# Kernel optimization log

Measured on AMD Instinct MI355X. Metric: run time of the kernel, lower is better.

## Reference

```python
import jax, jax.numpy as jnp
import numpy as np

N, E, B = 10000, 25000, 128
NF, EF, D = 32, 8, 64
STEPS = 3   # message passing steps
S2S = 3     # set2set processing steps
EPS = 1e-5

def setup_inputs() -> dict:
    key = jax.random.key(0)
    ks = jax.random.split(key, 32)
    g = lambda i, shape, scale=0.05: (jax.random.normal(ks[i], shape, dtype=jnp.float32) * scale)
    inp = {
        'x': jax.random.normal(ks[0], (N, NF), dtype=jnp.float32),
        'edge_index': jax.random.randint(ks[1], (2, E), 0, N, dtype=jnp.int32),
        'edge_attr': jax.random.normal(ks[2], (E, EF), dtype=jnp.float32),
        'batch': jnp.sort(jax.random.randint(ks[3], (N,), 0, B, dtype=jnp.int32)),
        # dense0
        'W0': g(4, (NF, D)), 'b0': jnp.zeros((D,), jnp.float32),
        # edge MLP: EF -> 2D -> D*D
        'We1': g(5, (EF, 2 * D)), 'be1': jnp.zeros((2 * D,), jnp.float32),
        'We2': g(6, (2 * D, D * D)), 'be2': jnp.zeros((D * D,), jnp.float32),
        # NNConv root weight + bias
        'root': g(7, (D, D)), 'conv_b': jnp.zeros((D,), jnp.float32),
        # GRU (input D, hidden D); gate order r, z, n (torch layout)
        'Wi': g(8, (D, 3 * D)), 'bi': jnp.zeros((3 * D,), jnp.float32),
        'Wh': g(9, (D, 3 * D)), 'bh': jnp.zeros((3 * D,), jnp.float32),
        # Set2Set LSTM (input 2D, hidden D); gate order i, f, g, o
        'Wli': g(10, (2 * D, 4 * D)), 'bli': jnp.zeros((4 * D,), jnp.float32),
        'Wlh': g(11, (D, 4 * D)), 'blh': jnp.zeros((4 * D,), jnp.float32),
        'Wr1': g(12, (2 * D, D)), 'br1': jnp.zeros((D,), jnp.float32),
        'gamma': jnp.ones((D,), jnp.float32), 'beta': jnp.zeros((D,), jnp.float32),
        'Wr2': g(13, (D, 1)), 'br2': jnp.zeros((1,), jnp.float32),
    }
    return inp

def _forward(x, edge_index, edge_attr, batch, W0, b0, We1, be1, We2, be2,
             root, conv_b, Wi, bi, Wh, bh, Wli, bli, Wlh, blh,
             Wr1, br1, gamma, beta, Wr2, br2):
    src, dst = edge_index[0], edge_index[1]
    out = jax.nn.relu(x @ W0 + b0)            # [N, D]
    h = out                                    # GRU hidden (seq_len=1)
    # edge-conditioned weights depend only on edge_attr -> compute once
    ew = (jax.nn.relu(edge_attr @ We1 + be1) @ We2 + be2).reshape(E, D, D)
    deg = jnp.maximum(jax.ops.segment_sum(jnp.ones((E,), x.dtype), dst, num_segments=N), 1.0)
    for _ in range(STEPS):
        msg = jnp.einsum('ed,edf->ef', out[src], ew)               # [E, D]
        agg = jax.ops.segment_sum(msg, dst, num_segments=N) / deg[:, None]
        m = jax.nn.relu(agg + out @ root + conv_b)                  # NNConv + relu
        # GRU cell
        gi = m @ Wi + bi
        gh = h @ Wh + bh
        ir, iz, ig = jnp.split(gi, 3, axis=-1)
        hr, hz, hg = jnp.split(gh, 3, axis=-1)
        r = jax.nn.sigmoid(ir + hr)
        z = jax.nn.sigmoid(iz + hz)
        n = jnp.tanh(ig + r * hg)
        h = (1.0 - z) * n + z * h
        out = h
    # Set2Set readout
    q_star = jnp.zeros((B, 2 * D), x.dtype)
    hl = jnp.zeros((B, D), x.dtype)
    cl = jnp.zeros((B, D), x.dtype)
    for _ in range(S2S):
        gates = q_star @ Wli + bli + hl @ Wlh + blh
        ig_, fg_, gg_, og_ = jnp.split(gates, 4, axis=-1)
        cl = jax.nn.sigmoid(fg_) * cl + jax.nn.sigmoid(ig_) * jnp.tanh(gg_)
        hl = jax.nn.sigmoid(og_) * jnp.tanh(cl)
        q = hl                                                      # [B, D]
        e = jnp.sum(out * q[batch], axis=-1)                        # [N]
        emax = jax.ops.segment_max(e, batch, num_segments=B)
        a = jnp.exp(e - emax[batch])
        a = a / jnp.maximum(jax.ops.segment_sum(a, batch, num_segments=B), 1e-12)[batch]
        r_read = jax.ops.segment_sum(a[:, None] * out, batch, num_segments=B)  # [B, D]
        q_star = jnp.concatenate([q, r_read], axis=-1)
    y = q_star @ Wr1 + br1
    mu = jnp.mean(y, axis=0)
    var = jnp.mean((y - mu) ** 2, axis=0)
    y = (y - mu) * jax.lax.rsqrt(var + EPS) * gamma + beta
    y = jax.nn.relu(y)
    y = y @ Wr2 + br2
    return y.reshape(-1)                                            # [B]

def reference(x, edge_index, edge_attr, batch, W0, b0, We1, be1, We2, be2,
              root, conv_b, Wi, bi, Wh, bh, Wli, bli, Wlh, blh,
              Wr1, br1, gamma, beta, Wr2, br2):
    return _forward(x, edge_index, edge_attr, batch, W0, b0, We1, be1, We2, be2,
                    root, conv_b, Wi, bi, Wh, bh, Wli, bli, Wlh, blh,
                    Wr1, br1, gamma, beta, Wr2, br2)
```

## Files before the change

### kernel.cpp

```cpp
#include <hip/hip_runtime.h>
#include <hip/hip_bf16.h>

constexpr int kN = 10000;
constexpr int kE = 25000;
constexpr int kB = 128;
constexpr int kNF = 32;
constexpr int kEF = 8;
constexpr int kD = 64;
constexpr int kGrp = 392;
constexpr int kEPad = kGrp * 64;
constexpr int kNCap = 320;

typedef __attribute__((ext_vector_type(8))) short short8;
typedef __attribute__((ext_vector_type(4))) float floatx4;
typedef __attribute__((ext_vector_type(16))) float floatx16;
typedef _Float16 half8 __attribute__((ext_vector_type(8)));

union HU { uint4 u; half8 h; short8 s; };

__device__ __forceinline__ unsigned short f2h(float f) {
  union { _Float16 h; unsigned short u; } cv;
  cv.h = (_Float16)f;
  return cv.u;
}
__device__ __forceinline__ unsigned pkrtz(float lo, float hi) {
  unsigned r;
  asm("v_cvt_pkrtz_f16_f32 %0, %1, %2" : "=v"(r) : "v"(lo), "v"(hi));
  return r;
}
__device__ __forceinline__ float sigmf(float x) { return 1.f / (1.f + __expf(-x)); }
__device__ __forceinline__ float tanh_(float x) { return 1.f - 2.f / (__expf(2.f * x) + 1.f); }

constexpr int kBlkDense = 2500;
constexpr int kBlkHid   = 12544;
constexpr int kBlkPrep  = 258;
constexpr int kBlkDeg   = 98;
constexpr int kB0H = kBlkDense;
constexpr int kB0P = kB0H + kBlkHid;
constexpr int kB0G = kB0P + kBlkPrep;
constexpr int kB0B = kB0G + kBlkDeg;
constexpr int kBlkSetup = kB0B + 1;

__global__ __launch_bounds__(256) void k_setup(
    const float* __restrict__ x, const float* __restrict__ W0, const float* __restrict__ b0,
    const float* __restrict__ ea, const float* __restrict__ We1, const float* __restrict__ be1,
    const float* __restrict__ We2, const float* __restrict__ be2,
    const int* __restrict__ ei, const int* __restrict__ batch,
    float* __restrict__ outn, unsigned short* __restrict__ hid7,
    unsigned short* __restrict__ Bc2, float* __restrict__ deg, int* __restrict__ start) {
  const int blk = blockIdx.x, t = threadIdx.x;
  if (blk < kB0H) {
    int gid = blk * 256 + t;
    int n = gid >> 6, f = gid & 63;
    float acc = b0[f];
    const float* xr = x + n * kNF;
#pragma unroll
    for (int j = 0; j < kNF; ++j) acc += xr[j] * W0[j * kD + f];
    outn[gid] = fmaxf(acc, 0.f);
  } else if (blk < kB0P) {
    int gid = (blk - kB0H) * 256 + t;
    int e_loc = gid & 63, h = (gid >> 6) & 127, grp = gid >> 13;
    int e = grp * 64 + e_loc;
    float r = 0.f;
    if (e < kE) {
      float acc = be1[h];
      const float* er = ea + e * kEF;
#pragma unroll
      for (int j = 0; j < kEF; ++j) acc += er[j] * We1[j * 128 + h];
      r = fmaxf(acc, 0.f);
    }
    hid7[gid] = f2h(r);
  } else if (blk < kB0G) {
    int lg = (blk - kB0P) * 256 + t;
    int lane = lg & 63, slot = lg >> 6;
    int fcol, dbase;
    const float* srcmat;
    if (slot < 1024) {
      int nf_ = slot & 1, hdb = slot >> 1;
      int db = hdb & 3, h = hdb >> 2;
      fcol = nf_ * 32 + (lane & 31);
      dbase = db * 16 + (lane >> 5) * 8;
      srcmat = We2 + (size_t)h * 4096;
    } else {
      int s = slot - 1024;
      int db = s >> 1, nf_ = s & 1;
      fcol = nf_ * 32 + (lane & 31);
      dbase = db * 16 + (lane >> 5) * 8;
      srcmat = be2;
    }
    unsigned short v[8];
#pragma unroll
    for (int j = 0; j < 8; ++j) v[j] = f2h(srcmat[(size_t)(dbase + j) * 64 + fcol]);
    *(short8*)(Bc2 + (size_t)slot * 512 + lane * 8) = *(short8*)v;
  } else if (blk < kB0B) {
    int e = (blk - kB0G) * 256 + t;
    if (e < kE) atomicAdd(&deg[ei[kE + e]], 1.f);
  } else {
    if (t > kB) return;
    int lo = 0, hi = kN;
    while (lo < hi) { int mid = (lo + hi) >> 1; if (batch[mid] < t) lo = mid + 1; else hi = mid; }
    start[t] = lo;
  }
}

__global__ __launch_bounds__(256) void k_csr(const float* __restrict__ deg,
                                             int* __restrict__ ptr) {
  __shared__ int ps[256];
  int t = threadIdx.x;
  int base = t * 40;
  int s = 0;
#pragma unroll 8
  for (int j = 0; j < 40; ++j) {
    int n = base + j;
    if (n < kN) s += (int)deg[n];
  }
  ps[t] = s;
  __syncthreads();
  for (int off = 1; off < 256; off <<= 1) {
    int v = (t >= off) ? ps[t - off] : 0;
    __syncthreads();
    ps[t] += v;
    __syncthreads();
  }
  int run = ps[t] - s;
  for (int j = 0; j < 40; ++j) {
    int n = base + j;
    if (n < kN) { ptr[n] = run; run += (int)deg[n]; }
  }
  if (t == 255) ptr[kN] = ps[255];
}

__global__ __launch_bounds__(256) void k_scatter(const int* __restrict__ ei,
    const int* __restrict__ ptr, int* __restrict__ cnt, int* __restrict__ perm) {
  int e = blockIdx.x * 256 + threadIdx.x;
  if (e < kE) {
    int d = ei[kE + e];
    int pos = atomicAdd(&cnt[d], 1);
    perm[e] = ptr[d] + pos;
  }
}

__global__ __launch_bounds__(256) void k_msgA(const int* __restrict__ ei,
    const float* __restrict__ outn, const unsigned short* __restrict__ hid7,
    const unsigned short* __restrict__ Bc2, const int* __restrict__ perm,
    float* __restrict__ msg0, float* __restrict__ msg1) {
  __shared__ __align__(16) unsigned short hidS[64 * 64];
  __shared__ __align__(16) float res[4][32 * 64];
  const int t = threadIdx.x, lane = t & 63, wave = t >> 6;
  const int er = lane & 31, hi5 = lane >> 5;
  const int grp = blockIdx.x, by = blockIdx.y, e0 = grp * 64;
  float* __restrict__ msgP = by ? msg1 : msg0;
  {
    const char* hsrc = (const char*)(hid7 + (size_t)grp * 8192 + by * 4096);
#pragma unroll
    for (int i = 0; i < 2; ++i) {
      int off = (wave * 2 + i) * 1024 + lane * 16;
      __builtin_amdgcn_global_load_lds(
          (const __attribute__((address_space(1))) void*)(hsrc + off),
          (__attribute__((address_space(3))) void*)((char*)hidS + off), 16, 0, 0);
    }
  }
  const int hg0 = by * 64 + wave * 16;
  const unsigned short* bp = Bc2 + (size_t)(hg0 * 8) * 512 + lane * 8;
  short8 bvr[8];
#pragma unroll
  for (int j = 0; j < 8; ++j) bvr[j] = *(const short8*)(bp + (size_t)j * 512);
  HU o8[2][4];
#pragma unroll
  for (int mf = 0; mf < 2; ++mf) {
    int e = e0 + mf * 32 + er;
    int s = (e < kE) ? ei[e] : 0;
    const float* base = outn + (size_t)s * 64 + hi5 * 8;
#pragma unroll
    for (int db = 0; db < 4; ++db) {
      floatx4 q0 = *(const floatx4*)(base + db * 16);
      floatx4 q1 = *(const floatx4*)(base + db * 16 + 4);
      o8[mf][db].u = (uint4){pkrtz(q0.x, q0.y), pkrtz(q0.z, q0.w),
                             pkrtz(q1.x, q1.y), pkrtz(q1.z, q1.w)};
    }
  }
  __syncthreads();

  floatx16 acc[2][2];
#pragma unroll
  for (int mf = 0; mf < 2; ++mf)
#pragma unroll
    for (int nf = 0; nf < 2; ++nf)
#pragma unroll
      for (int i = 0; i < 16; ++i) acc[mf][nf][i] = 0.f;

  const int hl0 = wave * 16;
#pragma unroll 2
  for (int hh = 0; hh < 16; ++hh) {
    int hl = hl0 + hh;
    unsigned p0 = (unsigned)hidS[hl * 64 + er] * 0x10001u;
    unsigned p1 = (unsigned)hidS[hl * 64 + 32 + er] * 0x10001u;
    HU hv0, hv1;
    hv0.u = (uint4){p0, p0, p0, p0};
    hv1.u = (uint4){p1, p1, p1, p1};
    const unsigned short* bpn = bp + (size_t)((hh + 1) * 8) * 512;
#pragma unroll
    for (int db = 0; db < 4; ++db) {
      HU bv0, bv1;
      bv0.s = bvr[db * 2]; bv1.s = bvr[db * 2 + 1];
      bvr[db * 2]     = *(const short8*)(bpn + (size_t)(db * 2) * 512);
      bvr[db * 2 + 1] = *(const short8*)(bpn + (size_t)(db * 2 + 1) * 512);
      half8 a0 = o8[0][db].h * hv0.h;
      half8 a1 = o8[1][db].h * hv1.h;
      acc[0][0] = __builtin_amdgcn_mfma_f32_32x32x16_f16(a0, bv0.h, acc[0][0], 0, 0, 0);
      acc[0][1] = __builtin_amdgcn_mfma_f32_32x32x16_f16(a0, bv1.h, acc[0][1], 0, 0, 0);
      acc[1][0] = __builtin_amdgcn_mfma_f32_32x32x16_f16(a1, bv0.h, acc[1][0], 0, 0, 0);
      acc[1][1] = __builtin_amdgcn_mfma_f32_32x32x16_f16(a1, bv1.h, acc[1][1], 0, 0, 0);
    }
  }
  if (by == 1 && wave == 3) {
#pragma unroll
    for (int db = 0; db < 4; ++db) {
      HU bv0, bv1;
      bv0.s = *(const short8*)(Bc2 + (size_t)(1024 + db * 2) * 512 + lane * 8);
      bv1.s = *(const short8*)(Bc2 + (size_t)(1024 + db * 2 + 1) * 512 + lane * 8);
      acc[0][0] = __builtin_amdgcn_mfma_f32_32x32x16_f16(o8[0][db].h, bv0.h, acc[0][0], 0, 0, 0);
      acc[0][1] = __builtin_amdgcn_mfma_f32_32x32x16_f16(o8[0][db].h, bv1.h, acc[0][1], 0, 0, 0);
      acc[1][0] = __builtin_amdgcn_mfma_f32_32x32x16_f16(o8[1][db].h, bv0.h, acc[1][0], 0, 0, 0);
      acc[1][1] = __builtin_amdgcn_mfma_f32_32x32x16_f16(o8[1][db].h, bv1.h, acc[1][1], 0, 0, 0);
    }
  }
#pragma unroll
  for (int mf = 0; mf < 2; ++mf) {
#pragma unroll
    for (int nf = 0; nf < 2; ++nf)
#pragma unroll
      for (int reg = 0; reg < 16; ++reg) {
        int row = (reg & 3) + 8 * (reg >> 2) + 4 * hi5;
        res[wave][row * 64 + nf * 32 + er] = acc[mf][nf][reg];
      }
    __syncthreads();
#pragma unroll
    for (int q = 0; q < 2; ++q) {
      int idx = q * 1024 + t * 4;
      float4 s4 = *(const float4*)&res[0][idx];
#pragma unroll
      for (int w = 1; w < 4; ++w) {
        float4 a4 = *(const float4*)&res[w][idx];
        s4.x += a4.x; s4.y += a4.y; s4.z += a4.z; s4.w += a4.w;
      }
      int e = e0 + mf * 32 + (idx >> 6);
      if (e < kE) {
        int pe = perm[e];
        *(float4*)(msgP + (size_t)pe * 64 + (idx & 63)) = s4;
      }
    }
    __syncthreads();
  }
}

__global__ __launch_bounds__(256) void k_update(const float* __restrict__ msg0,
    const float* __restrict__ msg1, const int* __restrict__ ptr,
    const float* __restrict__ deg,
    const float* __restrict__ root, const float* __restrict__ convb,
    const float* __restrict__ Wi, const float* __restrict__ bi,
    const float* __restrict__ Wh, const float* __restrict__ bh,
    float* __restrict__ out) {
  __shared__ float sh_out[8][64];
  __shared__ float sh_m[8][64];
  int t = threadIdx.x, lane = t & 63, w = t >> 6;
  int nb = blockIdx.x * 8;
#pragma unroll
  for (int i = 0; i < 2; ++i) {
    int idx = t + i * 256;
    sh_out[idx >> 6][idx & 63] = out[(size_t)(nb + (idx >> 6)) * 64 + (idx & 63)];
  }
  __syncthreads();
  int n0 = w * 2;
  float acc[2];
#pragma unroll
  for (int i = 0; i < 2; ++i) {
    int n = nb + n0 + i;
    float dg = fmaxf(deg[n], 1.f);
    float s = 0.f;
    int p0 = ptr[n], p1 = ptr[n + 1];
    for (int k = p0; k < p1; ++k) {
      size_t off2 = (size_t)k * 64 + lane;
      s += msg0[off2] + msg1[off2];
    }
    acc[i] = s / dg + convb[lane];
  }
  for (int d = 0; d < 64; ++d) {
    float rv = root[d * 64 + lane];
#pragma unroll
    for (int i = 0; i < 2; ++i) acc[i] += sh_out[n0 + i][d] * rv;
  }
#pragma unroll
  for (int i = 0; i < 2; ++i) sh_m[n0 + i][lane] = fmaxf(acc[i], 0.f);
  __syncthreads();
  float ir[2] = {}, iz[2] = {}, ig[2] = {}, hr[2] = {}, hz[2] = {}, hg[2] = {};
  for (int d = 0; d < 64; ++d) {
    float wi0 = Wi[d * 192 + lane], wi1 = Wi[d * 192 + 64 + lane], wi2 = Wi[d * 192 + 128 + lane];
    float wh0 = Wh[d * 192 + lane], wh1 = Wh[d * 192 + 64 + lane], wh2 = Wh[d * 192 + 128 + lane];
#pragma unroll
    for (int i = 0; i < 2; ++i) {
      float mv = sh_m[n0 + i][d], hv = sh_out[n0 + i][d];
      ir[i] += mv * wi0; iz[i] += mv * wi1; ig[i] += mv * wi2;
      hr[i] += hv * wh0; hz[i] += hv * wh1; hg[i] += hv * wh2;
    }
  }
  float bi0 = bi[lane], bi1 = bi[64 + lane], bi2 = bi[128 + lane];
  float bh0 = bh[lane], bh1 = bh[64 + lane], bh2 = bh[128 + lane];
#pragma unroll
  for (int i = 0; i < 2; ++i) {
    float r = sigmf(ir[i] + bi0 + hr[i] + bh0);
    float z = sigmf(iz[i] + bi1 + hz[i] + bh1);
    float nn = tanh_(ig[i] + bi2 + r * (hg[i] + bh2));
    float h = sh_out[n0 + i][lane];
    out[(size_t)(nb + n0 + i) * 64 + lane] = (1.f - z) * nn + z * h;
  }
}

__global__ __launch_bounds__(256) void k_s2s3(const float* __restrict__ out,
    const int* __restrict__ start, const float* __restrict__ Wli,
    const float* __restrict__ bli, const float* __restrict__ Wlh,
    const float* __restrict__ blh, const float* __restrict__ Wr1,
    const float* __restrict__ br1, float* __restrict__ y1) {
  __shared__ float sno[kNCap * 65];
  __shared__ float ebuf[1024];
  __shared__ float qs[128], hls[64], cls[64], gates[256];
  __shared__ float part[4][64];
  __shared__ float sred[8];
  int b = blockIdx.x, t = threadIdx.x, lane = t & 63, w = t >> 6;
  int s0 = start[b], s1 = start[b + 1];
  int cnt = s1 - s0; if (cnt > 1024) cnt = 1024;
  int cstg = cnt < kNCap ? cnt : kNCap;
  for (int i = t; i < cstg * 64; i += 256)
    sno[(i >> 6) * 65 + (i & 63)] = out[(size_t)(s0 + (i >> 6)) * 64 + (i & 63)];
  if (t < 128) qs[t] = 0.f;
  if (t < 64) { hls[t] = 0.f; cls[t] = 0.f; }
  __syncthreads();
  for (int it = 0; it < 3; ++it) {
    float g = bli[t] + blh[t];
    for (int j = 0; j < 128; ++j) g += qs[j] * Wli[j * 256 + t];
    for (int j = 0; j < 64; ++j) g += hls[j] * Wlh[j * 256 + t];
    gates[t] = g;
    __syncthreads();
    if (t < 64) {
      float ig = sigmf(gates[t]), fg = sigmf(gates[64 + t]);
      float gg = tanh_(gates[128 + t]), og = sigmf(gates[192 + t]);
      float c = fg * cls[t] + ig * gg;
      float h = og * tanh_(c);
      cls[t] = c; hls[t] = h;
      qs[t] = h;
    }
    __syncthreads();
    for (int n = t; n < cnt; n += 256) {
      float e = 0.f;
      if (n < kNCap) {
        const float* row = &sno[n * 65];
#pragma unroll 16
        for (int d = 0; d < 64; ++d) e += row[d] * hls[d];
      } else {
        const float* row = out + (size_t)(s0 + n) * 64;
        for (int d = 0; d < 64; ++d) e += row[d] * hls[d];
      }
      ebuf[n] = e;
    }
    __syncthreads();
    float mx = -3.4e38f;
    for (int idx = t; idx < cnt; idx += 256) mx = fmaxf(mx, ebuf[idx]);
#pragma unroll
    for (int m = 1; m < 64; m <<= 1) mx = fmaxf(mx, __shfl_xor(mx, m, 64));
    if (lane == 0) sred[w] = mx;
    __syncthreads();
    mx = fmaxf(fmaxf(sred[0], sred[1]), fmaxf(sred[2], sred[3]));
    float s = 0.f;
    for (int idx = t; idx < cnt; idx += 256) {
      float a = __expf(ebuf[idx] - mx);
      ebuf[idx] = a; s += a;
    }
#pragma unroll
    for (int m = 1; m < 64; m <<= 1) s += __shfl_xor(s, m, 64);
    if (lane == 0) sred[4 + w] = s;
    __syncthreads();
    s = sred[4] + sred[5] + sred[6] + sred[7];
    float rs = 1.f / fmaxf(s, 1e-12f);
    float pr = 0.f;
    for (int n = w; n < cnt; n += 4) {
      float a = ebuf[n];
      pr += a * ((n < kNCap) ? sno[n * 65 + lane] : out[(size_t)(s0 + n) * 64 + lane]);
    }
    part[w][lane] = pr;
    __syncthreads();
    if (t < 64)
      qs[64 + t] = (part[0][t] + part[1][t] + part[2][t] + part[3][t]) * rs;
    __syncthreads();
  }
  if (t < 64) {
    float acc = br1[t];
    for (int j = 0; j < 128; ++j) acc += qs[j] * Wr1[j * 64 + t];
    y1[b * 64 + t] = acc;
  }
}

__global__ __launch_bounds__(256) void k_head2(const float* __restrict__ y1,
    const float* __restrict__ gamma, const float* __restrict__ beta,
    const float* __restrict__ Wr2, const float* __restrict__ br2,
    float* __restrict__ outp) {
  __shared__ float mu[64], ri[64];
  int t = threadIdx.x;
  if (t < 64) {
    float s1 = 0.f, s2 = 0.f;
    for (int b = 0; b < kB; ++b) { float v = y1[b * 64 + t]; s1 += v; s2 += v * v; }
    float m = s1 / (float)kB;
    mu[t] = m; ri[t] = rsqrtf(s2 / (float)kB - m * m + 1e-5f);
  }
  __syncthreads();
  if (t < kB) {
    float acc = br2[0];
    for (int f = 0; f < 64; ++f) {
      float v = (y1[t * 64 + f] - mu[f]) * ri[f] * gamma[f] + beta[f];
      acc += fmaxf(v, 0.f) * Wr2[f];
    }
    outp[t] = acc;
  }
}

extern "C" void kernel_launch(void* const* d_in, const int* in_sizes, int n_in,
                              void* d_out, int out_size, void* d_ws, size_t ws_size,
                              hipStream_t stream) {
  const float* x     = (const float*)d_in[0];
  const int*   ei    = (const int*)d_in[1];
  const float* ea    = (const float*)d_in[2];
  const int*   batch = (const int*)d_in[3];
  const float* W0    = (const float*)d_in[4];
  const float* b0    = (const float*)d_in[5];
  const float* We1   = (const float*)d_in[6];
  const float* be1   = (const float*)d_in[7];
  const float* We2   = (const float*)d_in[8];
  const float* be2   = (const float*)d_in[9];
  const float* root  = (const float*)d_in[10];
  const float* convb = (const float*)d_in[11];
  const float* Wi    = (const float*)d_in[12];
  const float* bi    = (const float*)d_in[13];
  const float* Wh    = (const float*)d_in[14];
  const float* bh    = (const float*)d_in[15];
  const float* Wli   = (const float*)d_in[16];
  const float* bli   = (const float*)d_in[17];
  const float* Wlh   = (const float*)d_in[18];
  const float* blh   = (const float*)d_in[19];
  const float* Wr1   = (const float*)d_in[20];
  const float* br1   = (const float*)d_in[21];
  const float* gamma = (const float*)d_in[22];
  const float* beta  = (const float*)d_in[23];
  const float* Wr2   = (const float*)d_in[24];
  const float* br2   = (const float*)d_in[25];
  (void)in_sizes; (void)n_in; (void)out_size; (void)ws_size;

  char* ws = (char*)d_ws;
  size_t off = 0;
  auto take = [&](size_t bytes) {
    char* p = ws + off;
    off += (bytes + 255) & ~(size_t)255;
    return p;
  };
  float* deg  = (float*)take((size_t)kN * 4);
  int*   cnt  = (int*)take((size_t)kN * 4);
  size_t zeroBytes = off;
  int*   ptr   = (int*)take((size_t)(kN + 1) * 4);
  int*   perm  = (int*)take((size_t)kE * 4);
  int*   start = (int*)take(256 * 4);
  float* outn  = (float*)take((size_t)kN * kD * 4);
  float* msg0  = (float*)take((size_t)kEPad * kD * 4);
  float* msg1  = (float*)take((size_t)kEPad * kD * 4);
  unsigned short* hid7 = (unsigned short*)take((size_t)kGrp * 8192 * 2);
  unsigned short* Bc2  = (unsigned short*)take((size_t)1032 * 512 * 2);
  float* y1    = (float*)take((size_t)kB * 64 * 4);

  hipMemsetAsync(deg, 0, zeroBytes, stream);
  k_setup<<<kBlkSetup, 256, 0, stream>>>(x, W0, b0, ea, We1, be1, We2, be2, ei, batch,
                                         outn, hid7, Bc2, deg, start);
  k_csr<<<1, 256, 0, stream>>>(deg, ptr);
  k_scatter<<<(kE + 255) / 256, 256, 0, stream>>>(ei, ptr, cnt, perm);
  dim3 gm(kGrp, 2);
  for (int s = 0; s < 3; ++s) {
    k_msgA<<<gm, 256, 0, stream>>>(ei, outn, hid7, Bc2, perm, msg0, msg1);
    k_update<<<kN / 8, 256, 0, stream>>>(msg0, msg1, ptr, deg, root, convb,
                                         Wi, bi, Wh, bh, outn);
  }
  k_s2s3<<<kB, 256, 0, stream>>>(outn, start, Wli, bli, Wlh, blh, Wr1, br1, y1);
  k_head2<<<1, 256, 0, stream>>>(y1, gamma, beta, Wr2, br2, (float*)d_out);
}
```

Measured before the change: 270.4 us.

## Repartition message kernel: waves own edge rows, split hidden dim four ways

The message kernel now gives each wave its own 32 edges of a 128-edge group and splits the 128 hidden units across four grid-y slices. Each wave walks all 32 hidden units of its slice, so the cross-wave reduction through shared memory and its barriers go away, and each wave writes its accumulators straight to the permuted message rows. In exchange there are four partial message buffers that the update kernel must read and sum, and each wave streams the full B matrix slice per edge set. The per-edge global stores are now scalar rather than float4.

```diff
diff --git a/kernel.cpp b/kernel.cpp
--- a/kernel.cpp
+++ b/kernel.cpp
@@ -7,8 +7,8 @@
 constexpr int kNF = 32;
 constexpr int kEF = 8;
 constexpr int kD = 64;
-constexpr int kGrp = 392;
-constexpr int kEPad = kGrp * 64;
+constexpr int kGrp = 196;
+constexpr int kEPad = kGrp * 128;
 constexpr int kNCap = 320;
 
 typedef __attribute__((ext_vector_type(8))) short short8;
@@ -59,8 +59,8 @@
     outn[gid] = fmaxf(acc, 0.f);
   } else if (blk < kB0P) {
     int gid = (blk - kB0H) * 256 + t;
-    int e_loc = gid & 63, h = (gid >> 6) & 127, grp = gid >> 13;
-    int e = grp * 64 + e_loc;
+    int e_loc = gid & 127, h = (gid >> 7) & 127, grp = gid >> 14;
+    int e = grp * 128 + e_loc;
     float r = 0.f;
     if (e < kE) {
       float acc = be1[h];
@@ -143,15 +143,14 @@
 __global__ __launch_bounds__(256) void k_msgA(const int* __restrict__ ei,
     const float* __restrict__ outn, const unsigned short* __restrict__ hid7,
     const unsigned short* __restrict__ Bc2, const int* __restrict__ perm,
-    float* __restrict__ msg0, float* __restrict__ msg1) {
-  __shared__ __align__(16) unsigned short hidS[64 * 64];
-  __shared__ __align__(16) float res[4][32 * 64];
+    float* __restrict__ msg, size_t msgStride) {
+  __shared__ __align__(16) unsigned short hidS[32 * 128];
   const int t = threadIdx.x, lane = t & 63, wave = t >> 6;
   const int er = lane & 31, hi5 = lane >> 5;
-  const int grp = blockIdx.x, by = blockIdx.y, e0 = grp * 64;
-  float* __restrict__ msgP = by ? msg1 : msg0;
+  const int grp = blockIdx.x, qy = blockIdx.y, e0 = grp * 128;
+  float* __restrict__ msgP = msg + (size_t)qy * msgStride;
   {
-    const char* hsrc = (const char*)(hid7 + (size_t)grp * 8192 + by * 4096);
+    const char* hsrc = (const char*)(hid7 + (size_t)grp * 16384 + qy * 4096);
 #pragma unroll
     for (int i = 0; i < 2; ++i) {
       int off = (wave * 2 + i) * 1024 + lane * 16;
@@ -160,44 +159,34 @@
           (__attribute__((address_space(3))) void*)((char*)hidS + off), 16, 0, 0);
     }
   }
-  const int hg0 = by * 64 + wave * 16;
-  const unsigned short* bp = Bc2 + (size_t)(hg0 * 8) * 512 + lane * 8;
+  const unsigned short* bp = Bc2 + (size_t)(qy * 32 * 8) * 512 + lane * 8;
   short8 bvr[8];
 #pragma unroll
   for (int j = 0; j < 8; ++j) bvr[j] = *(const short8*)(bp + (size_t)j * 512);
-  HU o8[2][4];
-#pragma unroll
-  for (int mf = 0; mf < 2; ++mf) {
-    int e = e0 + mf * 32 + er;
+  HU o8[4];
+  {
+    int e = e0 + wave * 32 + er;
     int s = (e < kE) ? ei[e] : 0;
     const float* base = outn + (size_t)s * 64 + hi5 * 8;
 #pragma unroll
     for (int db = 0; db < 4; ++db) {
       floatx4 q0 = *(const floatx4*)(base + db * 16);
       floatx4 q1 = *(const floatx4*)(base + db * 16 + 4);
-      o8[mf][db].u = (uint4){pkrtz(q0.x, q0.y), pkrtz(q0.z, q0.w),
-                             pkrtz(q1.x, q1.y), pkrtz(q1.z, q1.w)};
-    }
-  }
-  __syncthreads();
-
-  floatx16 acc[2][2];
-#pragma unroll
-  for (int mf = 0; mf < 2; ++mf)
-#pragma unroll
-    for (int nf = 0; nf < 2; ++nf)
-#pragma unroll
-      for (int i = 0; i < 16; ++i) acc[mf][nf][i] = 0.f;
-
-  const int hl0 = wave * 16;
+      o8[db].u = (uint4){pkrtz(q0.x, q0.y), pkrtz(q0.z, q0.w),
+                         pkrtz(q1.x, q1.y), pkrtz(q1.z, q1.w)};
+    }
+  }
+  __syncthreads();
+
+  floatx16 acc[2];
+#pragma unroll
+  for (int i = 0; i < 16; ++i) { acc[0][i] = 0.f; acc[1][i] = 0.f; }
+
 #pragma unroll 2
-  for (int hh = 0; hh < 16; ++hh) {
-    int hl = hl0 + hh;
-    unsigned p0 = (unsigned)hidS[hl * 64 + er] * 0x10001u;
-    unsigned p1 = (unsigned)hidS[hl * 64 + 32 + er] * 0x10001u;
-    HU hv0, hv1;
-    hv0.u = (uint4){p0, p0, p0, p0};
-    hv1.u = (uint4){p1, p1, p1, p1};
+  for (int hh = 0; hh < 32; ++hh) {
+    unsigned p0 = (unsigned)hidS[hh * 128 + wave * 32 + er] * 0x10001u;
+    HU hv;
+    hv.u = (uint4){p0, p0, p0, p0};
     const unsigned short* bpn = bp + (size_t)((hh + 1) * 8) * 512;
 #pragma unroll
     for (int db = 0; db < 4; ++db) {
@@ -205,58 +194,35 @@
       bv0.s = bvr[db * 2]; bv1.s = bvr[db * 2 + 1];
       bvr[db * 2]     = *(const short8*)(bpn + (size_t)(db * 2) * 512);
       bvr[db * 2 + 1] = *(const short8*)(bpn + (size_t)(db * 2 + 1) * 512);
-      half8 a0 = o8[0][db].h * hv0.h;
-      half8 a1 = o8[1][db].h * hv1.h;
-      acc[0][0] = __builtin_amdgcn_mfma_f32_32x32x16_f16(a0, bv0.h, acc[0][0], 0, 0, 0);
-      acc[0][1] = __builtin_amdgcn_mfma_f32_32x32x16_f16(a0, bv1.h, acc[0][1], 0, 0, 0);
-      acc[1][0] = __builtin_amdgcn_mfma_f32_32x32x16_f16(a1, bv0.h, acc[1][0], 0, 0, 0);
-      acc[1][1] = __builtin_amdgcn_mfma_f32_32x32x16_f16(a1, bv1.h, acc[1][1], 0, 0, 0);
-    }
-  }
-  if (by == 1 && wave == 3) {
+      half8 a = o8[db].h * hv.h;
+      acc[0] = __builtin_amdgcn_mfma_f32_32x32x16_f16(a, bv0.h, acc[0], 0, 0, 0);
+      acc[1] = __builtin_amdgcn_mfma_f32_32x32x16_f16(a, bv1.h, acc[1], 0, 0, 0);
+    }
+  }
+  if (qy == 3) {
 #pragma unroll
     for (int db = 0; db < 4; ++db) {
       HU bv0, bv1;
       bv0.s = *(const short8*)(Bc2 + (size_t)(1024 + db * 2) * 512 + lane * 8);
       bv1.s = *(const short8*)(Bc2 + (size_t)(1024 + db * 2 + 1) * 512 + lane * 8);
-      acc[0][0] = __builtin_amdgcn_mfma_f32_32x32x16_f16(o8[0][db].h, bv0.h, acc[0][0], 0, 0, 0);
-      acc[0][1] = __builtin_amdgcn_mfma_f32_32x32x16_f16(o8[0][db].h, bv1.h, acc[0][1], 0, 0, 0);
-      acc[1][0] = __builtin_amdgcn_mfma_f32_32x32x16_f16(o8[1][db].h, bv0.h, acc[1][0], 0, 0, 0);
-      acc[1][1] = __builtin_amdgcn_mfma_f32_32x32x16_f16(o8[1][db].h, bv1.h, acc[1][1], 0, 0, 0);
-    }
-  }
-#pragma unroll
-  for (int mf = 0; mf < 2; ++mf) {
-#pragma unroll
-    for (int nf = 0; nf < 2; ++nf)
-#pragma unroll
-      for (int reg = 0; reg < 16; ++reg) {
-        int row = (reg & 3) + 8 * (reg >> 2) + 4 * hi5;
-        res[wave][row * 64 + nf * 32 + er] = acc[mf][nf][reg];
-      }
-    __syncthreads();
-#pragma unroll
-    for (int q = 0; q < 2; ++q) {
-      int idx = q * 1024 + t * 4;
-      float4 s4 = *(const float4*)&res[0][idx];
-#pragma unroll
-      for (int w = 1; w < 4; ++w) {
-        float4 a4 = *(const float4*)&res[w][idx];
-        s4.x += a4.x; s4.y += a4.y; s4.z += a4.z; s4.w += a4.w;
-      }
-      int e = e0 + mf * 32 + (idx >> 6);
-      if (e < kE) {
-        int pe = perm[e];
-        *(float4*)(msgP + (size_t)pe * 64 + (idx & 63)) = s4;
-      }
-    }
-    __syncthreads();
-  }
-}
-
-__global__ __launch_bounds__(256) void k_update(const float* __restrict__ msg0,
-    const float* __restrict__ msg1, const int* __restrict__ ptr,
-    const float* __restrict__ deg,
+      acc[0] = __builtin_amdgcn_mfma_f32_32x32x16_f16(o8[db].h, bv0.h, acc[0], 0, 0, 0);
+      acc[1] = __builtin_amdgcn_mfma_f32_32x32x16_f16(o8[db].h, bv1.h, acc[1], 0, 0, 0);
+    }
+  }
+#pragma unroll
+  for (int rg = 0; rg < 16; ++rg) {
+    int row = (rg & 3) + 8 * (rg >> 2) + 4 * hi5;
+    int e = e0 + wave * 32 + row;
+    if (e < kE) {
+      float* rp = msgP + (size_t)perm[e] * 64 + er;
+      rp[0]  = acc[0][rg];
+      rp[32] = acc[1][rg];
+    }
+  }
+}
+
+__global__ __launch_bounds__(256) void k_update(const float* __restrict__ msg,
+    size_t msgStride, const int* __restrict__ ptr, const float* __restrict__ deg,
     const float* __restrict__ root, const float* __restrict__ convb,
     const float* __restrict__ Wi, const float* __restrict__ bi,
     const float* __restrict__ Wh, const float* __restrict__ bh,
@@ -280,8 +246,8 @@
     float s = 0.f;
     int p0 = ptr[n], p1 = ptr[n + 1];
     for (int k = p0; k < p1; ++k) {
-      size_t off2 = (size_t)k * 64 + lane;
-      s += msg0[off2] + msg1[off2];
+      size_t o2 = (size_t)k * 64 + lane;
+      s += msg[o2] + msg[o2 + msgStride] + msg[o2 + 2 * msgStride] + msg[o2 + 3 * msgStride];
     }
     acc[i] = s / dg + convb[lane];
   }
@@ -467,9 +433,9 @@
   int*   perm  = (int*)take((size_t)kE * 4);
   int*   start = (int*)take(256 * 4);
   float* outn  = (float*)take((size_t)kN * kD * 4);
-  float* msg0  = (float*)take((size_t)kEPad * kD * 4);
-  float* msg1  = (float*)take((size_t)kEPad * kD * 4);
-  unsigned short* hid7 = (unsigned short*)take((size_t)kGrp * 8192 * 2);
+  const size_t msgStride = (size_t)kEPad * kD;
+  float* msg  = (float*)take(4 * msgStride * 4);
+  unsigned short* hid7 = (unsigned short*)take((size_t)kGrp * 16384 * 2);
   unsigned short* Bc2  = (unsigned short*)take((size_t)1032 * 512 * 2);
   float* y1    = (float*)take((size_t)kB * 64 * 4);
 
@@ -478,10 +444,10 @@
                                          outn, hid7, Bc2, deg, start);
   k_csr<<<1, 256, 0, stream>>>(deg, ptr);
   k_scatter<<<(kE + 255) / 256, 256, 0, stream>>>(ei, ptr, cnt, perm);
-  dim3 gm(kGrp, 2);
+  dim3 gm(kGrp, 4);
   for (int s = 0; s < 3; ++s) {
-    k_msgA<<<gm, 256, 0, stream>>>(ei, outn, hid7, Bc2, perm, msg0, msg1);
-    k_update<<<kN / 8, 256, 0, stream>>>(msg0, msg1, ptr, deg, root, convb,
+    k_msgA<<<gm, 256, 0, stream>>>(ei, outn, hid7, Bc2, perm, msg, msgStride);
+    k_update<<<kN / 8, 256, 0, stream>>>(msg, msgStride, ptr, deg, root, convb,
                                          Wi, bi, Wh, bh, outn);
   }
   k_s2s3<<<kB, 256, 0, stream>>>(outn, start, Wli, bli, Wlh, blh, Wr1, br1, y1);
```

New measurement: 284.6 us. 5.3% more time.

## Merge split-K message blocks into one 512-thread block with single output buffer

Applied to the files above, without the earlier changes.

The message kernel previously split the hidden dimension across two blocks (blockIdx.y), each writing partial sums to separate msg0/msg1 buffers that k_update then added. Now one 512-thread block with 8 waves covers the full reduction, sums all eight partials in shared memory, and writes a single msg buffer. This halves the message write and read traffic and removes the extra load in the update gather. The cost is double the shared memory per block (16 KB hid plus 64 KB res) and half as many blocks, which may lower occupancy.

```diff
diff --git a/kernel.cpp b/kernel.cpp
--- a/kernel.cpp
+++ b/kernel.cpp
@@ -140,18 +140,17 @@
   }
 }
 
-__global__ __launch_bounds__(256) void k_msgA(const int* __restrict__ ei,
+__global__ __launch_bounds__(512) void k_msgB(const int* __restrict__ ei,
     const float* __restrict__ outn, const unsigned short* __restrict__ hid7,
     const unsigned short* __restrict__ Bc2, const int* __restrict__ perm,
-    float* __restrict__ msg0, float* __restrict__ msg1) {
-  __shared__ __align__(16) unsigned short hidS[64 * 64];
-  __shared__ __align__(16) float res[4][32 * 64];
+    float* __restrict__ msg) {
+  __shared__ __align__(16) unsigned short hidS[128 * 64];
+  __shared__ __align__(16) float res[8][32 * 64];
   const int t = threadIdx.x, lane = t & 63, wave = t >> 6;
   const int er = lane & 31, hi5 = lane >> 5;
-  const int grp = blockIdx.x, by = blockIdx.y, e0 = grp * 64;
-  float* __restrict__ msgP = by ? msg1 : msg0;
+  const int grp = blockIdx.x, e0 = grp * 64;
   {
-    const char* hsrc = (const char*)(hid7 + (size_t)grp * 8192 + by * 4096);
+    const char* hsrc = (const char*)(hid7 + (size_t)grp * 8192);
 #pragma unroll
     for (int i = 0; i < 2; ++i) {
       int off = (wave * 2 + i) * 1024 + lane * 16;
@@ -160,8 +159,7 @@
           (__attribute__((address_space(3))) void*)((char*)hidS + off), 16, 0, 0);
     }
   }
-  const int hg0 = by * 64 + wave * 16;
-  const unsigned short* bp = Bc2 + (size_t)(hg0 * 8) * 512 + lane * 8;
+  const unsigned short* bp = Bc2 + (size_t)(wave * 128) * 512 + lane * 8;
   short8 bvr[8];
 #pragma unroll
   for (int j = 0; j < 8; ++j) bvr[j] = *(const short8*)(bp + (size_t)j * 512);
@@ -213,7 +211,7 @@
       acc[1][1] = __builtin_amdgcn_mfma_f32_32x32x16_f16(a1, bv1.h, acc[1][1], 0, 0, 0);
     }
   }
-  if (by == 1 && wave == 3) {
+  if (wave == 7) {
 #pragma unroll
     for (int db = 0; db < 4; ++db) {
       HU bv0, bv1;
@@ -235,28 +233,26 @@
         res[wave][row * 64 + nf * 32 + er] = acc[mf][nf][reg];
       }
     __syncthreads();
-#pragma unroll
-    for (int q = 0; q < 2; ++q) {
-      int idx = q * 1024 + t * 4;
+    {
+      int idx = t * 4;
       float4 s4 = *(const float4*)&res[0][idx];
 #pragma unroll
-      for (int w = 1; w < 4; ++w) {
+      for (int w = 1; w < 8; ++w) {
         float4 a4 = *(const float4*)&res[w][idx];
         s4.x += a4.x; s4.y += a4.y; s4.z += a4.z; s4.w += a4.w;
       }
       int e = e0 + mf * 32 + (idx >> 6);
       if (e < kE) {
         int pe = perm[e];
-        *(float4*)(msgP + (size_t)pe * 64 + (idx & 63)) = s4;
+        *(float4*)(msg + (size_t)pe * 64 + (idx & 63)) = s4;
       }
     }
     __syncthreads();
   }
 }
 
-__global__ __launch_bounds__(256) void k_update(const float* __restrict__ msg0,
-    const float* __restrict__ msg1, const int* __restrict__ ptr,
-    const float* __restrict__ deg,
+__global__ __launch_bounds__(256) void k_update(const float* __restrict__ msg,
+    const int* __restrict__ ptr, const float* __restrict__ deg,
     const float* __restrict__ root, const float* __restrict__ convb,
     const float* __restrict__ Wi, const float* __restrict__ bi,
     const float* __restrict__ Wh, const float* __restrict__ bh,
@@ -279,10 +275,8 @@
     float dg = fmaxf(deg[n], 1.f);
     float s = 0.f;
     int p0 = ptr[n], p1 = ptr[n + 1];
-    for (int k = p0; k < p1; ++k) {
-      size_t off2 = (size_t)k * 64 + lane;
-      s += msg0[off2] + msg1[off2];
-    }
+    for (int k = p0; k < p1; ++k)
+      s += msg[(size_t)k * 64 + lane];
     acc[i] = s / dg + convb[lane];
   }
   for (int d = 0; d < 64; ++d) {
@@ -467,8 +461,7 @@
   int*   perm  = (int*)take((size_t)kE * 4);
   int*   start = (int*)take(256 * 4);
   float* outn  = (float*)take((size_t)kN * kD * 4);
-  float* msg0  = (float*)take((size_t)kEPad * kD * 4);
-  float* msg1  = (float*)take((size_t)kEPad * kD * 4);
+  float* msg   = (float*)take((size_t)kEPad * kD * 4);
   unsigned short* hid7 = (unsigned short*)take((size_t)kGrp * 8192 * 2);
   unsigned short* Bc2  = (unsigned short*)take((size_t)1032 * 512 * 2);
   float* y1    = (float*)take((size_t)kB * 64 * 4);
@@ -478,10 +471,9 @@
                                          outn, hid7, Bc2, deg, start);
   k_csr<<<1, 256, 0, stream>>>(deg, ptr);
   k_scatter<<<(kE + 255) / 256, 256, 0, stream>>>(ei, ptr, cnt, perm);
-  dim3 gm(kGrp, 2);
   for (int s = 0; s < 3; ++s) {
-    k_msgA<<<gm, 256, 0, stream>>>(ei, outn, hid7, Bc2, perm, msg0, msg1);
-    k_update<<<kN / 8, 256, 0, stream>>>(msg0, msg1, ptr, deg, root, convb,
+    k_msgB<<<kGrp, 512, 0, stream>>>(ei, outn, hid7, Bc2, perm, msg);
+    k_update<<<kN / 8, 256, 0, stream>>>(msg, ptr, deg, root, convb,
                                          Wi, bi, Wh, bh, outn);
   }
   k_s2s3<<<kB, 256, 0, stream>>>(outn, start, Wli, bli, Wlh, blh, Wr1, br1, y1);
```

Result: no change. 273.0 us (+1.0%).
